# Kernel tuning notes

Hardware: AMD Instinct MI355X
Metric: run time of the kernel (lower is better)

## Reference

```python
import jax, jax.numpy as jnp
import numpy as np

B, T, C = 4, 2048, 1024


def setup_inputs() -> dict:
    key = jax.random.key(0)
    ks = jax.random.split(key, 5)
    s = 1.0 / np.sqrt(C)
    return {
        "X": jax.random.normal(ks[0], (B, T, C), dtype=jnp.float32),
        "Wq": jax.random.normal(ks[1], (C, C), dtype=jnp.float32) * s,
        "Wk": jax.random.normal(ks[2], (C, C), dtype=jnp.float32) * s,
        "Wv": jax.random.normal(ks[3], (C, C), dtype=jnp.float32) * s,
        "Wo": jax.random.normal(ks[4], (C, C), dtype=jnp.float32) * s,
    }


def reference(X, Wq, Wk, Wv, Wo):
    Bx, Tx, Cx = X.shape
    Q = X @ Wq  # [B,T,C]
    K = X @ Wk
    V = X @ Wv
    scores = jnp.einsum('btc,bsc->bts', Q, K) / jnp.sqrt(jnp.asarray(Cx, X.dtype))
    # causal mask: position t attends to s <= t
    causal = jnp.tril(jnp.ones((Tx, Tx), dtype=bool))
    scores = jnp.where(causal, scores, jnp.asarray(-jnp.inf, scores.dtype))
    weights = jax.nn.softmax(scores, axis=-1)
    out = jnp.einsum('bts,bsc->btc', weights, V)
    return out @ Wo
```

## Files before the change

### kernel.cpp

```cpp
#include <hip/hip_runtime.h>
#include <hip/hip_bf16.h>
#include <cmath>


typedef __attribute__((ext_vector_type(8))) __bf16 bf16x8;
typedef __attribute__((ext_vector_type(8))) short short8;
typedef __attribute__((ext_vector_type(4))) float f32x4;

__device__ __forceinline__ unsigned short f2bf(float f) {
  union { float f; unsigned u; } v; v.f = f;
  unsigned u = v.u;
  u += ((u >> 16) & 1u) + 0x7fffu;
  return (unsigned short)(u >> 16);
}
__device__ __forceinline__ float bf2f(unsigned short h) {
  union { unsigned u; float f; } v; v.u = ((unsigned)h) << 16;
  return v.f;
}

#define GLDS(gp, sp)                                                           \
  __builtin_amdgcn_global_load_lds(                                            \
      (const __attribute__((address_space(1))) void*)(gp),                     \
      (__attribute__((address_space(3))) void*)(sp), 16, 0, 0)

__global__ void prep(const float* __restrict__ X,
                     const float* __restrict__ w0, const float* __restrict__ w1,
                     const float* __restrict__ w2, const float* __restrict__ w3,
                     unsigned short* __restrict__ Xb,
                     unsigned short* __restrict__ wcat,
                     unsigned short* __restrict__ wvb,
                     unsigned short* __restrict__ wot,
                     int n) {
  if (blockIdx.z == 2) {
    int bx = blockIdx.x * 32, by = blockIdx.y * 32;
    int tx = threadIdx.x, ty = threadIdx.y;
#pragma unroll
    for (int i = 0; i < 32; i += 8) {
      size_t idx = (size_t)(by + ty + i) * n + bx + tx;
      wvb[idx] = f2bf(w2[idx]);
    }
  } else if (blockIdx.z < 4) {
    const float* src = blockIdx.z == 0 ? w0 : blockIdx.z == 1 ? w1 : w3;
    unsigned short* dst = blockIdx.z == 0 ? wcat
                          : blockIdx.z == 1 ? wcat + (size_t)n * n : wot;
    __shared__ float tile[32][33];
    int bx = blockIdx.x * 32, by = blockIdx.y * 32;
    int tx = threadIdx.x, ty = threadIdx.y;
#pragma unroll
    for (int i = 0; i < 32; i += 8)
      tile[ty + i][tx] = src[(size_t)(by + ty + i) * n + bx + tx];
    __syncthreads();
#pragma unroll
    for (int i = 0; i < 32; i += 8)
      dst[(size_t)(bx + ty + i) * n + by + tx] = f2bf(tile[tx][ty + i]);
  } else {
    const int bid = (blockIdx.z - 4) * 1024 + blockIdx.y * 32 + blockIdx.x;
    const int t = threadIdx.y * 32 + threadIdx.x;
    const int i = (bid * 256 + t) * 4;
    float4 f = *(const float4*)(X + i);
    ushort4 o = make_ushort4(f2bf(f.x), f2bf(f.y), f2bf(f.z), f2bf(f.w));
    *(ushort4*)(Xb + i) = o;
  }
}

template <typename OutT, int NW>
__global__ __launch_bounds__(NW * 64, NW / 2)
void gemm_bt(const unsigned short* __restrict__ A, int lda, long long sA,
             const unsigned short* __restrict__ B, int ldb, long long sB,
             OutT* __restrict__ Cp, int ldc, long long sC,
             int K, float alpha, int tri, int kcap, int gx) {
  A  += (long long)blockIdx.z * sA;
  B  += (long long)blockIdx.z * sB;
  Cp += (long long)blockIdx.z * sC;

  int by, bx;
  if (tri) {
    int idx = blockIdx.x;
    idx = (idx & 7) * ((int)gridDim.x >> 3) + (idx >> 3);
    by = (int)((sqrtf(8.f * idx + 1.f) - 1.f) * 0.5f);
    while (by * (by + 1) / 2 > idx) --by;
    while ((by + 1) * (by + 2) / 2 <= idx) ++by;
    bx = idx - by * (by + 1) / 2;
  } else if (gx > 0) {
    const int id = blockIdx.x;
    const int gs = gx * 8;
    const int g = id / gs, r = id - g * gs;
    bx = r >> 3;
    by = g * 8 + (r & 7);
    if (kcap) by = (gridDim.x / gx) - 1 - by;
  } else {
    by = blockIdx.y;
    bx = blockIdx.x;
  }
  const int m0 = by * 128;
  const int n0 = bx * 128;
  const int Keff = kcap ? min(K, m0 + 128) : K;

  const int tid  = threadIdx.x;
  const int lane = tid & 63;
  const int w    = tid >> 6;
  const int wm   = (NW == 4) ? (w >> 1) * 64 : (w >> 1) * 32;
  const int wn   = (w & 1) * 64;
  const int quad = lane >> 4;
  const int l16  = lane & 15;
  constexpr int AI = (NW == 4) ? 4 : 2;
  constexpr int NR = 128 / (NW * 8);

  __shared__ unsigned short As[8192];
  __shared__ unsigned short Bs[8192];

  f32x4 acc[AI][4];
#pragma unroll
  for (int i = 0; i < AI; ++i)
#pragma unroll
    for (int j = 0; j < 4; ++j)
      acc[i][j] = (f32x4){0.f, 0.f, 0.f, 0.f};

  const int srow = tid >> 3;
  const int scol = ((tid & 7) ^ (srow & 7)) * 8;
  const unsigned short* gA = A + (long long)(m0 + srow) * lda + scol;
  const unsigned short* gB = B + (long long)(n0 + srow) * ldb + scol;
  const int rsw = l16 & 7;

  for (int kt = 0; kt < Keff; kt += 64) {
    __syncthreads();
#pragma unroll
    for (int r = 0; r < NR; ++r) {
      GLDS(gA + (long long)(r * NW * 8) * lda + kt, As + r * NW * 512 + tid * 8);
      GLDS(gB + (long long)(r * NW * 8) * ldb + kt, Bs + r * NW * 512 + tid * 8);
    }
    __syncthreads();
#pragma unroll
    for (int ks = 0; ks < 2; ++ks) {
      bf16x8 af[AI], bfr[4];
#pragma unroll
      for (int i = 0; i < AI; ++i)
        af[i] = *(const bf16x8*)(As + (wm + i * 16 + l16) * 64 +
                                 ((ks * 4 + quad) ^ rsw) * 8);
#pragma unroll
      for (int j = 0; j < 4; ++j)
        bfr[j] = *(const bf16x8*)(Bs + (wn + j * 16 + l16) * 64 +
                                  ((ks * 4 + quad) ^ rsw) * 8);
#pragma unroll
      for (int i = 0; i < AI; ++i)
#pragma unroll
        for (int j = 0; j < 4; ++j)
          acc[i][j] = __builtin_amdgcn_mfma_f32_16x16x32_bf16(af[i], bfr[j],
                                                              acc[i][j], 0, 0, 0);
    }
  }

#pragma unroll
  for (int i = 0; i < AI; ++i) {
#pragma unroll
    for (int j = 0; j < 4; ++j) {
      const int row = m0 + wm + i * 16 + quad * 4;
      const int col = n0 + wn + j * 16 + l16;
#pragma unroll
      for (int r = 0; r < 4; ++r) {
        float v = acc[i][j][r] * alpha;
        if constexpr (sizeof(OutT) == 2)
          Cp[(long long)(row + r) * ldc + col] = (OutT)f2bf(v);
        else
          Cp[(long long)(row + r) * ldc + col] = v;
      }
    }
  }
}

__global__ __launch_bounds__(256, 2)
void gemm_wvo(const unsigned short* __restrict__ A,
              const unsigned short* __restrict__ B,
              unsigned short* __restrict__ Cp, int n) {
  const int m0 = blockIdx.y * 64;
  const int n0 = blockIdx.x * 64;

  const int tid  = threadIdx.x;
  const int lane = tid & 63;
  const int w    = tid >> 6;
  const int wm   = (w >> 1) * 32;
  const int wn   = (w & 1) * 32;
  const int quad = lane >> 4;
  const int l16  = lane & 15;
  const int rsw  = l16 & 7;

  __shared__ unsigned short As[4096];
  __shared__ unsigned short Bs[4096];

  f32x4 acc[2][2];
#pragma unroll
  for (int i = 0; i < 2; ++i)
#pragma unroll
    for (int j = 0; j < 2; ++j)
      acc[i][j] = (f32x4){0.f, 0.f, 0.f, 0.f};

  const int srow = tid >> 3;
  const int scol = ((tid & 7) ^ (srow & 7)) * 8;
  const unsigned short* gA = A + (long long)(m0 + srow) * n + scol;
  const unsigned short* gB = B + (long long)(n0 + srow) * n + scol;

  for (int kt = 0; kt < n; kt += 64) {
    __syncthreads();
#pragma unroll
    for (int r = 0; r < 2; ++r) {
      GLDS(gA + (long long)(r * 32) * n + kt, As + r * 2048 + tid * 8);
      GLDS(gB + (long long)(r * 32) * n + kt, Bs + r * 2048 + tid * 8);
    }
    __syncthreads();
#pragma unroll
    for (int ks = 0; ks < 2; ++ks) {
      bf16x8 af[2], bfr[2];
#pragma unroll
      for (int i = 0; i < 2; ++i)
        af[i] = *(const bf16x8*)(As + (wm + i * 16 + l16) * 64 +
                                 ((ks * 4 + quad) ^ rsw) * 8);
#pragma unroll
      for (int j = 0; j < 2; ++j)
        bfr[j] = *(const bf16x8*)(Bs + (wn + j * 16 + l16) * 64 +
                                  ((ks * 4 + quad) ^ rsw) * 8);
#pragma unroll
      for (int i = 0; i < 2; ++i)
#pragma unroll
        for (int j = 0; j < 2; ++j)
          acc[i][j] = __builtin_amdgcn_mfma_f32_16x16x32_bf16(af[i], bfr[j],
                                                              acc[i][j], 0, 0, 0);
    }
  }

#pragma unroll
  for (int i = 0; i < 2; ++i) {
#pragma unroll
    for (int j = 0; j < 2; ++j) {
      const int row = m0 + wm + i * 16 + quad * 4;
      const int col = n0 + wn + j * 16 + l16;
#pragma unroll
      for (int r = 0; r < 4; ++r)
        Cp[(long long)(row + r) * n + col] = f2bf(acc[i][j][r]);
    }
  }
}

__global__ __launch_bounds__(256, 2)
void gemm_qkv(const unsigned short* __restrict__ A, int lda,
              const unsigned short* __restrict__ B, int ldb,
              unsigned short* __restrict__ Cp, int K, int gx) {
  const int id = blockIdx.x;
  const int gs = gx * 8;
  const int g = id / gs, r = id - g * gs;
  const int bx = r >> 3;
  const int by = g * 8 + (r & 7);
  const int m0 = by * 128;
  const int n0 = bx * 128;

  const int tid  = threadIdx.x;
  const int lane = tid & 63;
  const int w    = tid >> 6;
  const int wm   = (w >> 1) * 64;
  const int wn   = (w & 1) * 64;
  const int quad = lane >> 4;
  const int l16  = lane & 15;

  __shared__ unsigned short As[8192];
  __shared__ unsigned short Bs[8192];

  f32x4 acc[4][4];
#pragma unroll
  for (int i = 0; i < 4; ++i)
#pragma unroll
    for (int j = 0; j < 4; ++j)
      acc[i][j] = (f32x4){0.f, 0.f, 0.f, 0.f};

  const int srow = tid >> 3;
  const int scol = ((tid & 7) ^ (srow & 7)) * 8;
  const unsigned short* gA = A + (long long)(m0 + srow) * lda + scol;
  const unsigned short* gB = B + (long long)(n0 + srow) * ldb + scol;
  const int rsw = l16 & 7;

  for (int kt = 0; kt < K; kt += 64) {
    __syncthreads();
#pragma unroll
    for (int r2 = 0; r2 < 4; ++r2) {
      GLDS(gA + (long long)(r2 * 32) * lda + kt, As + r2 * 2048 + tid * 8);
      GLDS(gB + (long long)(r2 * 32) * ldb + kt, Bs + r2 * 2048 + tid * 8);
    }
    __syncthreads();
#pragma unroll
    for (int ks = 0; ks < 2; ++ks) {
      bf16x8 af[4], bfr[4];
#pragma unroll
      for (int i = 0; i < 4; ++i)
        af[i] = *(const bf16x8*)(As + (wm + i * 16 + l16) * 64 +
                                 ((ks * 4 + quad) ^ rsw) * 8);
#pragma unroll
      for (int j = 0; j < 4; ++j)
        bfr[j] = *(const bf16x8*)(Bs + (wn + j * 16 + l16) * 64 +
                                  ((ks * 4 + quad) ^ rsw) * 8);
#pragma unroll
      for (int i = 0; i < 4; ++i)
#pragma unroll
        for (int j = 0; j < 4; ++j)
          acc[i][j] = __builtin_amdgcn_mfma_f32_16x16x32_bf16(af[i], bfr[j],
                                                              acc[i][j], 0, 0, 0);
    }
  }

#pragma unroll
  for (int i = 0; i < 4; ++i) {
#pragma unroll
    for (int j = 0; j < 4; ++j) {
      const int row = m0 + wm + i * 16 + quad * 4;
      const int col = n0 + wn + j * 16 + l16;
      if (col >= 2048) {
        const int b = row >> 11, t = row & 2047, cv = col - 2048;
        ushort4 o = make_ushort4(f2bf(acc[i][j][0]), f2bf(acc[i][j][1]),
                                 f2bf(acc[i][j][2]), f2bf(acc[i][j][3]));
        *(ushort4*)(Cp + 16777216LL + ((long long)(b * 1024 + cv)) * 2048 + t) = o;
      } else {
        unsigned short* dst = Cp + (col >= 1024 ? 8388608LL - 1024 : 0);
#pragma unroll
        for (int r2 = 0; r2 < 4; ++r2)
          dst[(long long)(row + r2) * 1024 + col] = f2bf(acc[i][j][r2]);
      }
    }
  }
}

__global__ __launch_bounds__(256)
void softmax_causal(const unsigned short* __restrict__ Sin,
                    unsigned short* __restrict__ Sout, int T) {
  const long long row = blockIdx.x;
  const int t = (int)(row & (long long)(T - 1));
  const int limit = ((t >> 7) + 1) << 7;
  const unsigned short* pin = Sin + row * T;
  unsigned short* pout = Sout + row * T;
  const int tid  = threadIdx.x;
  const int base = tid * 8;
  const bool active = base < limit;

  short8 raw = {};
  if (active) raw = *(const short8*)(pin + base);
  float x[8];
  float mx = -1e30f;
#pragma unroll
  for (int j = 0; j < 8; ++j) {
    bool valid = active && (base + j) <= t;
    x[j] = valid ? bf2f((unsigned short)raw[j]) : -1e30f;
    mx = fmaxf(mx, x[j]);
  }
#pragma unroll
  for (int off = 32; off > 0; off >>= 1) mx = fmaxf(mx, __shfl_xor(mx, off));
  __shared__ float red[8];
  const int wv = tid >> 6;
  if ((tid & 63) == 0) red[wv] = mx;
  __syncthreads();
  mx = fmaxf(fmaxf(red[0], red[1]), fmaxf(red[2], red[3]));

  float sum = 0.f;
#pragma unroll
  for (int j = 0; j < 8; ++j) {
    bool valid = active && (base + j) <= t;
    x[j] = valid ? __expf(x[j] - mx) : 0.f;
    sum += x[j];
  }
#pragma unroll
  for (int off = 32; off > 0; off >>= 1) sum += __shfl_xor(sum, off);
  if ((tid & 63) == 0) red[4 + wv] = sum;
  __syncthreads();
  sum = red[4] + red[5] + red[6] + red[7];
  const float inv = 1.f / sum;

  if (active) {
    unsigned short out[8];
#pragma unroll
    for (int j = 0; j < 8; ++j) out[j] = f2bf(x[j] * inv);
    *(short8*)(pout + base) = *(const short8*)out;
  }
}

extern "C" void kernel_launch(void* const* d_in, const int* in_sizes, int n_in,
                              void* d_out, int out_size, void* d_ws,
                              size_t ws_size, hipStream_t stream) {
  (void)in_sizes; (void)n_in; (void)out_size; (void)ws_size;
  const int Bb = 4, T = 2048, C = 1024;
  const int M = Bb * T;

  const float* X  = (const float*)d_in[0];
  const float* Wq = (const float*)d_in[1];
  const float* Wk = (const float*)d_in[2];
  const float* Wv = (const float*)d_in[3];
  const float* Wo = (const float*)d_in[4];

  char* w = (char*)d_ws;
  unsigned short* Wcat = (unsigned short*)w; w += (size_t)3 * C * C * 2;
  unsigned short* Q    = (unsigned short*)w; w += (size_t)M * C * 2;
  unsigned short* Kb   = (unsigned short*)w; w += (size_t)M * C * 2;
  unsigned short* Vt   = (unsigned short*)w; w += (size_t)M * C * 2;
  unsigned short* Xb   = (unsigned short*)w; w += (size_t)M * C * 2;
  (void)Kb;
  unsigned short* Wvb  = (unsigned short*)d_out;
  unsigned short* Wot  = (unsigned short*)d_out + (size_t)C * C;
  unsigned short* S    = (unsigned short*)d_out;
  unsigned short* Sn   = Q;

  prep<<<dim3(32, 32, 12), dim3(32, 8), 0, stream>>>(X, Wq, Wk, Wv, Wo, Xb,
                                                     Wcat, Wvb, Wot, C);

  gemm_wvo<<<dim3(C / 64, C / 64), dim3(256), 0, stream>>>(
      Wot, Wvb, Wcat + (size_t)2 * C * C, C);

  gemm_qkv<<<dim3((3 * C / 128) * (M / 128)), dim3(256), 0, stream>>>(
      Xb, C, Wcat, C, Q, C, 3 * C / 128);

  const int ntri = (T / 128) * (T / 128 + 1) / 2;
  gemm_bt<unsigned short, 8><<<dim3(ntri, 1, Bb), dim3(512), 0, stream>>>(
      Q, C, (long long)T * C, Kb, C, (long long)T * C,
      S, T, (long long)T * T, C, 0.03125f, 1, 0, 0);

  softmax_causal<<<M, 256, 0, stream>>>(S, Sn, T);

  gemm_bt<float, 8><<<dim3((C / 128) * (T / 128), 1, Bb), dim3(512), 0, stream>>>(
      Sn, T, (long long)T * T, Vt, T, (long long)C * T,
      (float*)d_out, C, (long long)T * C, T, 1.f, 0, 1, C / 128);
}
```

Measured before the change: 239.2 us.

## Fuse causal softmax into QK^T epilogue and PV row-sum normalisation

Removes the standalone softmax kernel. The QK^T GEMM epilogue now writes unnormalised exp(score) values, with the causal mask applied, to a workspace buffer. The PV GEMM sums each row of the bf16 probability tiles as they stream through registers and divides its output by that sum. This drops a full read and write pass over the T×T score matrix. The cost is that the max subtraction is gone, so exp can overflow if scores grow large, and every column tile of the PV GEMM recomputes the same row sums.

```diff
diff --git a/kernel.cpp b/kernel.cpp
--- a/kernel.cpp
+++ b/kernel.cpp
@@ -63,7 +63,7 @@
   }
 }
 
-template <typename OutT, int NW>
+template <typename OutT, int NW, int MODE>
 __global__ __launch_bounds__(NW * 64, NW / 2)
 void gemm_bt(const unsigned short* __restrict__ A, int lda, long long sA,
              const unsigned short* __restrict__ B, int ldb, long long sB,
@@ -116,6 +116,10 @@
     for (int j = 0; j < 4; ++j)
       acc[i][j] = (f32x4){0.f, 0.f, 0.f, 0.f};
 
+  float rsm[AI];
+#pragma unroll
+  for (int i = 0; i < AI; ++i) rsm[i] = 0.f;
+
   const int srow = tid >> 3;
   const int scol = ((tid & 7) ^ (srow & 7)) * 8;
   const unsigned short* gA = A + (long long)(m0 + srow) * lda + scol;
@@ -141,6 +145,14 @@
       for (int j = 0; j < 4; ++j)
         bfr[j] = *(const bf16x8*)(Bs + (wn + j * 16 + l16) * 64 +
                                   ((ks * 4 + quad) ^ rsw) * 8);
+      if constexpr (MODE == 2) {
+#pragma unroll
+        for (int i = 0; i < AI; ++i) {
+          short8 sv = __builtin_bit_cast(short8, af[i]);
+#pragma unroll
+          for (int e = 0; e < 8; ++e) rsm[i] += bf2f((unsigned short)sv[e]);
+        }
+      }
 #pragma unroll
       for (int i = 0; i < AI; ++i)
 #pragma unroll
@@ -150,19 +162,56 @@
     }
   }
 
-#pragma unroll
-  for (int i = 0; i < AI; ++i) {
-#pragma unroll
-    for (int j = 0; j < 4; ++j) {
+  if constexpr (MODE == 1) {
+#pragma unroll
+    for (int i = 0; i < AI; ++i) {
+#pragma unroll
+      for (int j = 0; j < 4; ++j) {
+        const int row = m0 + wm + i * 16 + quad * 4;
+        const int col = n0 + wn + j * 16 + l16;
+#pragma unroll
+        for (int r = 0; r < 4; ++r) {
+          float e = (col <= row + r) ? __expf(acc[i][j][r] * alpha) : 0.f;
+          Cp[(long long)(row + r) * ldc + col] = (OutT)f2bf(e);
+        }
+      }
+    }
+  } else if constexpr (MODE == 2) {
+#pragma unroll
+    for (int i = 0; i < AI; ++i) {
+      rsm[i] += __shfl_xor(rsm[i], 16);
+      rsm[i] += __shfl_xor(rsm[i], 32);
+    }
+#pragma unroll
+    for (int i = 0; i < AI; ++i) {
       const int row = m0 + wm + i * 16 + quad * 4;
-      const int col = n0 + wn + j * 16 + l16;
-#pragma unroll
-      for (int r = 0; r < 4; ++r) {
-        float v = acc[i][j][r] * alpha;
-        if constexpr (sizeof(OutT) == 2)
-          Cp[(long long)(row + r) * ldc + col] = (OutT)f2bf(v);
-        else
-          Cp[(long long)(row + r) * ldc + col] = v;
+      float inv[4];
+#pragma unroll
+      for (int r = 0; r < 4; ++r)
+        inv[r] = 1.f / __shfl(rsm[i], quad * 4 + r);
+#pragma unroll
+      for (int j = 0; j < 4; ++j) {
+        const int col = n0 + wn + j * 16 + l16;
+#pragma unroll
+        for (int r = 0; r < 4; ++r)
+          Cp[(long long)(row + r) * ldc + col] = acc[i][j][r] * inv[r];
+      }
+    }
+  } else {
+#pragma unroll
+    for (int i = 0; i < AI; ++i) {
+#pragma unroll
+      for (int j = 0; j < 4; ++j) {
+        const int row = m0 + wm + i * 16 + quad * 4;
+        const int col = n0 + wn + j * 16 + l16;
+#pragma unroll
+        for (int r = 0; r < 4; ++r) {
+          float v = acc[i][j][r] * alpha;
+          if constexpr (sizeof(OutT) == 2)
+            Cp[(long long)(row + r) * ldc + col] = (OutT)f2bf(v);
+          else
+            Cp[(long long)(row + r) * ldc + col] = v;
+        }
       }
     }
   }
@@ -243,7 +292,8 @@
 __global__ __launch_bounds__(256, 2)
 void gemm_qkv(const unsigned short* __restrict__ A, int lda,
               const unsigned short* __restrict__ B, int ldb,
-              unsigned short* __restrict__ Cp, int K, int gx) {
+              unsigned short* __restrict__ Cqk,
+              unsigned short* __restrict__ Cvt, int K, int gx) {
   const int id = blockIdx.x;
   const int gs = gx * 8;
   const int g = id / gs, r = id - g * gs;
@@ -314,66 +364,14 @@
         const int b = row >> 11, t = row & 2047, cv = col - 2048;
         ushort4 o = make_ushort4(f2bf(acc[i][j][0]), f2bf(acc[i][j][1]),
                                  f2bf(acc[i][j][2]), f2bf(acc[i][j][3]));
-        *(ushort4*)(Cp + 16777216LL + ((long long)(b * 1024 + cv)) * 2048 + t) = o;
+        *(ushort4*)(Cvt + ((long long)(b * 1024 + cv)) * 2048 + t) = o;
       } else {
-        unsigned short* dst = Cp + (col >= 1024 ? 8388608LL - 1024 : 0);
+        unsigned short* dst = Cqk + (col >= 1024 ? 8388608LL - 1024 : 0);
 #pragma unroll
         for (int r2 = 0; r2 < 4; ++r2)
           dst[(long long)(row + r2) * 1024 + col] = f2bf(acc[i][j][r2]);
       }
     }
-  }
-}
-
-__global__ __launch_bounds__(256)
-void softmax_causal(const unsigned short* __restrict__ Sin,
-                    unsigned short* __restrict__ Sout, int T) {
-  const long long row = blockIdx.x;
-  const int t = (int)(row & (long long)(T - 1));
-  const int limit = ((t >> 7) + 1) << 7;
-  const unsigned short* pin = Sin + row * T;
-  unsigned short* pout = Sout + row * T;
-  const int tid  = threadIdx.x;
-  const int base = tid * 8;
-  const bool active = base < limit;
-
-  short8 raw = {};
-  if (active) raw = *(const short8*)(pin + base);
-  float x[8];
-  float mx = -1e30f;
-#pragma unroll
-  for (int j = 0; j < 8; ++j) {
-    bool valid = active && (base + j) <= t;
-    x[j] = valid ? bf2f((unsigned short)raw[j]) : -1e30f;
-    mx = fmaxf(mx, x[j]);
-  }
-#pragma unroll
-  for (int off = 32; off > 0; off >>= 1) mx = fmaxf(mx, __shfl_xor(mx, off));
-  __shared__ float red[8];
-  const int wv = tid >> 6;
-  if ((tid & 63) == 0) red[wv] = mx;
-  __syncthreads();
-  mx = fmaxf(fmaxf(red[0], red[1]), fmaxf(red[2], red[3]));
-
-  float sum = 0.f;
-#pragma unroll
-  for (int j = 0; j < 8; ++j) {
-    bool valid = active && (base + j) <= t;
-    x[j] = valid ? __expf(x[j] - mx) : 0.f;
-    sum += x[j];
-  }
-#pragma unroll
-  for (int off = 32; off > 0; off >>= 1) sum += __shfl_xor(sum, off);
-  if ((tid & 63) == 0) red[4 + wv] = sum;
-  __syncthreads();
-  sum = red[4] + red[5] + red[6] + red[7];
-  const float inv = 1.f / sum;
-
-  if (active) {
-    unsigned short out[8];
-#pragma unroll
-    for (int j = 0; j < 8; ++j) out[j] = f2bf(x[j] * inv);
-    *(short8*)(pout + base) = *(const short8*)out;
   }
 }
 
@@ -392,15 +390,13 @@
 
   char* w = (char*)d_ws;
   unsigned short* Wcat = (unsigned short*)w; w += (size_t)3 * C * C * 2;
-  unsigned short* Q    = (unsigned short*)w; w += (size_t)M * C * 2;
-  unsigned short* Kb   = (unsigned short*)w; w += (size_t)M * C * 2;
+  unsigned short* Pp   = (unsigned short*)w; w += (size_t)M * T * 2;
   unsigned short* Vt   = (unsigned short*)w; w += (size_t)M * C * 2;
   unsigned short* Xb   = (unsigned short*)w; w += (size_t)M * C * 2;
-  (void)Kb;
-  unsigned short* Wvb  = (unsigned short*)d_out;
-  unsigned short* Wot  = (unsigned short*)d_out + (size_t)C * C;
-  unsigned short* S    = (unsigned short*)d_out;
-  unsigned short* Sn   = Q;
+  unsigned short* Wvb = (unsigned short*)d_out;
+  unsigned short* Wot = (unsigned short*)d_out + (size_t)C * C;
+  unsigned short* Qd  = (unsigned short*)d_out;
+  unsigned short* Kd  = Qd + (size_t)M * C;
 
   prep<<<dim3(32, 32, 12), dim3(32, 8), 0, stream>>>(X, Wq, Wk, Wv, Wo, Xb,
                                                      Wcat, Wvb, Wot, C);
@@ -409,16 +405,14 @@
       Wot, Wvb, Wcat + (size_t)2 * C * C, C);
 
   gemm_qkv<<<dim3((3 * C / 128) * (M / 128)), dim3(256), 0, stream>>>(
-      Xb, C, Wcat, C, Q, C, 3 * C / 128);
+      Xb, C, Wcat, C, Qd, Vt, C, 3 * C / 128);
 
   const int ntri = (T / 128) * (T / 128 + 1) / 2;
-  gemm_bt<unsigned short, 8><<<dim3(ntri, 1, Bb), dim3(512), 0, stream>>>(
-      Q, C, (long long)T * C, Kb, C, (long long)T * C,
-      S, T, (long long)T * T, C, 0.03125f, 1, 0, 0);
-
-  softmax_causal<<<M, 256, 0, stream>>>(S, Sn, T);
-
-  gemm_bt<float, 8><<<dim3((C / 128) * (T / 128), 1, Bb), dim3(512), 0, stream>>>(
-      Sn, T, (long long)T * T, Vt, T, (long long)C * T,
+  gemm_bt<unsigned short, 8, 1><<<dim3(ntri, 1, Bb), dim3(512), 0, stream>>>(
+      Qd, C, (long long)T * C, Kd, C, (long long)T * C,
+      Pp, T, (long long)T * T, C, 0.03125f, 1, 0, 0);
+
+  gemm_bt<float, 8, 2><<<dim3((C / 128) * (T / 128), 1, Bb), dim3(512), 0, stream>>>(
+      Pp, T, (long long)T * T, Vt, T, (long long)C * T,
       (float*)d_out, C, (long long)T * C, T, 1.f, 0, 1, C / 128);
 }
```

Result: slower. 244.7 us (+2.3%).
